# Kernel tuning notes

Hardware: AMD Instinct MI355X
Metric: run time of the kernel (lower is better)

The kernel has to match this reference:

```python
import jax, jax.numpy as jnp
import numpy as np

N_SRC = 50000
N_DST = 50000
N_EDGES = 1600000
D_IN = 128
K = 8          # num_heads
D_OUT = 16     # out_dim per head (K*D_OUT = 128)
NEG_SLOPE = 0.2


def setup_inputs() -> dict:
    key = jax.random.key(0)
    ks = jax.random.split(key, 8)
    feat_src = jax.random.normal(ks[0], (N_SRC, D_IN), dtype=jnp.float32)
    feat_dst = jax.random.normal(ks[1], (N_DST, D_IN), dtype=jnp.float32)
    W_src = jax.random.normal(ks[2], (D_IN, K * D_OUT), dtype=jnp.float32) * (1.0 / np.sqrt(D_IN))
    b_src = jnp.zeros((K * D_OUT,), dtype=jnp.float32)
    W_dst = jax.random.normal(ks[3], (D_IN, K * D_OUT), dtype=jnp.float32) * (1.0 / np.sqrt(D_IN))
    b_dst = jnp.zeros((K * D_OUT,), dtype=jnp.float32)
    attn_src = jax.random.normal(ks[4], (K, 2 * D_OUT), dtype=jnp.float32) * 0.1
    src_idx = jax.random.randint(ks[5], (N_EDGES,), 0, N_SRC, dtype=jnp.int64)
    dst_idx = jax.random.randint(ks[6], (N_EDGES,), 0, N_DST, dtype=jnp.int64)
    return {"feat_src": feat_src, "feat_dst": feat_dst, "W_src": W_src, "b_src": b_src,
            "W_dst": W_dst, "b_dst": b_dst, "attn_src": attn_src,
            "src_idx": src_idx, "dst_idx": dst_idx}


def reference(feat_src, feat_dst, W_src, b_src, W_dst, b_dst, attn_src, src_idx, dst_idx):
    n_dst = feat_dst.shape[0]
    # feat_drop is identity (p=0). Linear projections, reshape to heads.
    hs = (feat_src @ W_src + b_src).reshape(-1, K, D_OUT)  # [N_src, K, D_out]
    hd = (feat_dst @ W_dst + b_dst).reshape(-1, K, D_OUT)  # [N_dst, K, D_out]
    # per-node attention logits
    el = jnp.sum(hs * attn_src[:, :D_OUT], axis=-1)  # [N_src, K]
    er = jnp.sum(hd * attn_src[:, D_OUT:], axis=-1)  # [N_dst, K]
    # per-edge score: u_add_v then LeakyReLU
    e = el[src_idx] + er[dst_idx]                    # [E, K]
    e = jnp.where(e >= 0, e, NEG_SLOPE * e)
    # edge softmax over incoming edges of each dst node (numerically stable)
    emax = jax.ops.segment_max(e, dst_idx, num_segments=n_dst)
    emax = jnp.where(jnp.isfinite(emax), emax, 0.0)  # handle dsts with no edges
    ee = jnp.exp(e - emax[dst_idx])                  # [E, K]
    esum = jax.ops.segment_sum(ee, dst_idx, num_segments=n_dst)
    a = ee / esum[dst_idx]                           # [E, K]
    # weighted message aggregation: u_mul_e then sum over incoming edges
    m = hs[src_idx] * a[:, :, None]                  # [E, K, D_out]
    out = jax.ops.segment_sum(m, dst_idx, num_segments=n_dst)  # [N_dst, K, D_out]
    return out.reshape(n_dst, K * D_OUT)
```

## Files before the change

### kernel.cpp

```cpp
#include <hip/hip_runtime.h>
#include <hip/hip_bf16.h>

#define NEG_SLOPE 0.2f
#define EPB  8192
#define MAXC 2048

typedef __attribute__((ext_vector_type(8))) short bf16x8;
typedef __attribute__((ext_vector_type(4))) float f32x4;

__device__ __forceinline__ float b2f_lo(unsigned u) { return __uint_as_float(u << 16); }
__device__ __forceinline__ float b2f_hi(unsigned u) { return __uint_as_float(u & 0xffff0000u); }

__device__ __forceinline__ short f2b(float x) {
    unsigned u = __float_as_uint(x);
    unsigned r = (u + 0x7fffu + ((u >> 16) & 1u)) >> 16;
    return (short)r;
}

__global__ __launch_bounds__(256) void pack_kernel(
    const float* __restrict__ W_src, const float* __restrict__ W_dst,
    const float* __restrict__ b_src, const float* __restrict__ b_dst,
    const float* __restrict__ attn,
    uint4* __restrict__ wp_src, uint4* __restrict__ wp_dst,
    float* __restrict__ c_all)
{
    const int e = blockIdx.x * 256 + threadIdx.x;
    if (e < 4608) {
        const int which = e / 2304;
        const int e2 = e % 2304;
        const float* W = which ? W_dst : W_src;
        uint4* wp = which ? wp_dst : wp_src;
        const int aoff = which ? 16 : 0;
        short out[8];
        if (e2 < 2048) {
            const int t = e2 >> 8, q = (e2 >> 6) & 3, l = e2 & 63;
            const int kbase = (l >> 4) * 8 + q * 32;
            const int n = t * 16 + (l & 15);
            #pragma unroll
            for (int j = 0; j < 8; ++j) out[j] = f2b(W[(size_t)(kbase + j) * 128 + n]);
            *(uint4*)&wp[(t * 4 + q) * 64 + l] = *(uint4*)out;
        } else {
            const int e3 = e2 - 2048;
            const int q = e3 >> 6, l = e3 & 63;
            const int kbase = (l >> 4) * 8 + q * 32;
            const int n = l & 15;
            #pragma unroll
            for (int j = 0; j < 8; ++j) {
                float v = 0.f;
                if (n < 8) {
                    for (int dd = 0; dd < 16; ++dd)
                        v += W[(size_t)(kbase + j) * 128 + n * 16 + dd] * attn[n * 32 + aoff + dd];
                }
                out[j] = f2b(v);
            }
            *(uint4*)&wp[(32 + q) * 64 + l] = *(uint4*)out;
        }
    } else if (e < 4624) {
        const int k = e - 4608;
        const int which = k >> 3, kk = k & 7;
        const float* bb = which ? b_dst : b_src;
        const int aoff = which ? 16 : 0;
        float v = 0.f;
        for (int dd = 0; dd < 16; ++dd) v += bb[kk * 16 + dd] * attn[kk * 32 + aoff + dd];
        c_all[k] = v;
    }
}

__device__ __forceinline__ void hist_body(
    const int* __restrict__ dst_idx, int* __restrict__ Hmat,
    int nEdges, int nCoarse, int nCB, int bx)
{
    __shared__ int h[MAXC];
    const int t = threadIdx.x;
    for (int i = t; i < nCoarse; i += 256) h[i] = 0;
    __syncthreads();
    const int e0 = bx * EPB;
    const int e1 = min(e0 + EPB, nEdges);
    for (int e = e0 + t; e < e1; e += 256) atomicAdd(&h[dst_idx[e] >> 5], 1);
    __syncthreads();
    for (int i = t; i < nCoarse; i += 256) Hmat[(size_t)i * nCB + bx] = h[i];
}

template<bool STORE_H>
__device__ __forceinline__ void proj_body(
    const float* __restrict__ feat, const uint4* __restrict__ wp,
    const float* __restrict__ b, const float* __restrict__ cvec,
    short* __restrict__ hs_out, float* __restrict__ el_out,
    int N, int bx)
{
    const int t = threadIdx.x;
    const int lane = t & 63;
    const int w = t >> 6;
    const int m  = lane & 15;
    const int q8 = lane >> 4;
    const int row0 = bx * 128 + w * 32;

    f32x4 acc0[9], acc1[9];
    #pragma unroll
    for (int tt = 0; tt < 8; ++tt) {
        const float bn = b[tt * 16 + m];
        acc0[tt] = (f32x4){bn, bn, bn, bn};
        acc1[tt] = (f32x4){bn, bn, bn, bn};
    }
    acc0[8] = (f32x4){0.f, 0.f, 0.f, 0.f};
    acc1[8] = (f32x4){0.f, 0.f, 0.f, 0.f};

    int rowA0 = row0 + m;      if (rowA0 >= N) rowA0 = N - 1;
    int rowA1 = row0 + 16 + m; if (rowA1 >= N) rowA1 = N - 1;
    const float* f0 = feat + (size_t)rowA0 * 128 + q8 * 8;
    const float* f1 = feat + (size_t)rowA1 * 128 + q8 * 8;
    const bf16x8* wpv = (const bf16x8*)wp;

    #pragma unroll
    for (int kc = 0; kc < 4; ++kc) {
        const float4 fa0 = *(const float4*)(f0 + kc * 32);
        const float4 fb0 = *(const float4*)(f0 + kc * 32 + 4);
        const float4 fa1 = *(const float4*)(f1 + kc * 32);
        const float4 fb1 = *(const float4*)(f1 + kc * 32 + 4);
        bf16x8 a0, a1;
        a0[0]=f2b(fa0.x); a0[1]=f2b(fa0.y); a0[2]=f2b(fa0.z); a0[3]=f2b(fa0.w);
        a0[4]=f2b(fb0.x); a0[5]=f2b(fb0.y); a0[6]=f2b(fb0.z); a0[7]=f2b(fb0.w);
        a1[0]=f2b(fa1.x); a1[1]=f2b(fa1.y); a1[2]=f2b(fa1.z); a1[3]=f2b(fa1.w);
        a1[4]=f2b(fb1.x); a1[5]=f2b(fb1.y); a1[6]=f2b(fb1.z); a1[7]=f2b(fb1.w);
        #pragma unroll
        for (int tt = 0; tt < 8; ++tt) {
            const bf16x8 bf = wpv[(tt * 4 + kc) * 64 + lane];
            acc0[tt] = __builtin_amdgcn_mfma_f32_16x16x32_bf16(a0, bf, acc0[tt], 0, 0, 0);
            acc1[tt] = __builtin_amdgcn_mfma_f32_16x16x32_bf16(a1, bf, acc1[tt], 0, 0, 0);
        }
        {
            const bf16x8 bv = wpv[(32 + kc) * 64 + lane];
            acc0[8] = __builtin_amdgcn_mfma_f32_16x16x32_bf16(a0, bv, acc0[8], 0, 0, 0);
            acc1[8] = __builtin_amdgcn_mfma_f32_16x16x32_bf16(a1, bv, acc1[8], 0, 0, 0);
        }
    }

    #pragma unroll
    for (int half = 0; half < 2; ++half) {
        const f32x4* acc = half ? acc1 : acc0;
        const int rbase = row0 + half * 16 + q8 * 4;
        #pragma unroll
        for (int reg = 0; reg < 4; ++reg) {
            const int row = rbase + reg;
            if (row < N) {
                if (STORE_H) {
                    #pragma unroll
                    for (int tt = 0; tt < 8; ++tt)
                        hs_out[(size_t)row * 128 + tt * 16 + m] = f2b(acc[tt][reg]);
                }
                if (m < 8) el_out[(size_t)row * 8 + m] = acc[8][reg] + cvec[m];
            }
        }
    }
}

__global__ __launch_bounds__(256, 2) void fused_proj_hist_kernel(
    const float* __restrict__ feat_src, const float* __restrict__ feat_dst,
    const uint4* __restrict__ wp_src, const uint4* __restrict__ wp_dst,
    const float* __restrict__ b_src, const float* __restrict__ b_dst,
    const float* __restrict__ c_all,
    short* __restrict__ hs, float* __restrict__ el, float* __restrict__ er,
    const int* __restrict__ dst_idx, int* __restrict__ Hmat,
    int n_src, int n_dst, int nEdges, int nCoarse, int nCB, int pSrcBlocks)
{
    int bx = blockIdx.x;
    if (bx < nCB) { hist_body(dst_idx, Hmat, nEdges, nCoarse, nCB, bx); return; }
    bx -= nCB;
    if (bx < pSrcBlocks) {
        proj_body<true>(feat_src, wp_src, b_src, c_all, hs, el, n_src, bx);
        return;
    }
    bx -= pSrcBlocks;
    proj_body<false>(feat_dst, wp_dst, b_dst, c_all + 8, nullptr, er, n_dst, bx);
}

__global__ __launch_bounds__(1024) void scan_part_kernel(
    const int* __restrict__ cnt, int* __restrict__ part, int n)
{
    __shared__ int wsum[16];
    const int t = threadIdx.x;
    const int i = blockIdx.x * 1024 + t;
    int v = (i < n) ? cnt[i] : 0;
    #pragma unroll
    for (int s = 32; s > 0; s >>= 1) v += __shfl_down(v, s, 64);
    if ((t & 63) == 0) wsum[t >> 6] = v;
    __syncthreads();
    if (t < 16) {
        int x = wsum[t];
        #pragma unroll
        for (int s = 8; s > 0; s >>= 1) x += __shfl_down(x, s, 64);
        if (t == 0) part[blockIdx.x] = x;
    }
}

__global__ __launch_bounds__(1024) void scan_top_kernel(
    int* __restrict__ part, int* __restrict__ S, int nPart, int n)
{
    __shared__ int buf[1024];
    const int t = threadIdx.x;
    const int v = (t < nPart) ? part[t] : 0;
    buf[t] = v;
    __syncthreads();
    #pragma unroll
    for (int s = 1; s < 1024; s <<= 1) {
        const int add = (t >= s) ? buf[t - s] : 0;
        __syncthreads();
        buf[t] += add;
        __syncthreads();
    }
    if (t < nPart) part[t] = buf[t] - v;
    if (t == 1023) S[n] = buf[1023];
}

__global__ __launch_bounds__(1024) void scan_local_kernel(
    const int* __restrict__ cnt, const int* __restrict__ part,
    int* __restrict__ S, int n)
{
    __shared__ int buf[1024];
    const int t = threadIdx.x;
    const int i = blockIdx.x * 1024 + t;
    const int v = (i < n) ? cnt[i] : 0;
    buf[t] = v;
    __syncthreads();
    #pragma unroll
    for (int s = 1; s < 1024; s <<= 1) {
        const int add = (t >= s) ? buf[t - s] : 0;
        __syncthreads();
        buf[t] += add;
        __syncthreads();
    }
    if (i < n) S[i] = part[blockIdx.x] + buf[t] - v;
}

__global__ __launch_bounds__(256) void coarse_scatter_kernel(
    const int* __restrict__ src_idx, const int* __restrict__ dst_idx,
    const int* __restrict__ S, int* __restrict__ coarse,
    int nEdges, int nCoarse, int nCB)
{
    __shared__ int base_s[MAXC];
    __shared__ int cur_s[MAXC];
    const int t = threadIdx.x, bx = blockIdx.x;
    for (int i = t; i < nCoarse; i += 256) {
        base_s[i] = S[(size_t)i * nCB + bx];
        cur_s[i]  = 0;
    }
    __syncthreads();
    const int e0 = bx * EPB;
    const int e1 = min(e0 + EPB, nEdges);
    for (int e = e0 + t; e < e1; e += 256) {
        const int d = dst_idx[e];
        const int s = src_idx[e];
        const int bin = d >> 5;
        const int lr = atomicAdd(&cur_s[bin], 1);
        coarse[base_s[bin] + lr] = (s << 5) | (d & 31);
    }
}

__global__ __launch_bounds__(256) void fine_sort_kernel(
    const int* __restrict__ coarse, const int* __restrict__ S,
    int* __restrict__ off, int* __restrict__ sorted_src,
    int nEdges, int n_dst, int nCoarse, int nCB)
{
    __shared__ int h[32];
    __shared__ int cu[32];
    const int t = threadIdx.x, c = blockIdx.x;
    const int base = S[(size_t)c * nCB];
    const int endp = (c + 1 < nCoarse) ? S[(size_t)(c + 1) * nCB] : nEdges;
    if (t < 32) h[t] = 0;
    __syncthreads();
    for (int i = base + t; i < endp; i += 256) atomicAdd(&h[coarse[i] & 31], 1);
    __syncthreads();
    if (t == 0) {
        int run = 0;
        #pragma unroll
        for (int j = 0; j < 32; ++j) {
            cu[j] = run;
            const int d = c * 32 + j;
            if (d < n_dst) off[d] = base + run;
            run += h[j];
        }
    }
    __syncthreads();
    for (int i = base + t; i < endp; i += 256) {
        const int v = coarse[i];
        const int p = atomicAdd(&cu[v & 31], 1);
        sorted_src[base + p] = v >> 5;
    }
    if (c == 0 && t == 0) off[n_dst] = nEdges;
}

__global__ __launch_bounds__(256) void reduce_kernel(
    const int* __restrict__ sorted_src, const int* __restrict__ off,
    const __hip_bfloat16* __restrict__ hs,
    const float* __restrict__ el,
    const float* __restrict__ er,
    float* __restrict__ out,
    int n_dst)
{
    const int wid = blockIdx.x * 4 + (threadIdx.x >> 6);
    if (wid >= n_dst) return;
    const int lane = threadIdx.x & 63;
    const int sub  = lane >> 5;
    const int l32  = lane & 31;
    const int k    = l32 >> 2;
    const float erk = er[(size_t)wid * 8 + k];
    const int beg = off[wid], end = off[wid + 1];

    float a0 = 0.f, a1 = 0.f, a2 = 0.f, a3 = 0.f, es = 0.f;
    int i = beg + sub;
    for (; i + 2 < end; i += 4) {
        const int sA = sorted_src[i];
        const int sB = sorted_src[i + 2];
        const float lA = el[(size_t)sA * 8 + k];
        const float lB = el[(size_t)sB * 8 + k];
        const uint2 uA = ((const uint2*)(hs + (size_t)sA * 128))[l32];
        const uint2 uB = ((const uint2*)(hs + (size_t)sB * 128))[l32];
        float xA = lA + erk; xA = (xA >= 0.f) ? xA : NEG_SLOPE * xA;
        float xB = lB + erk; xB = (xB >= 0.f) ? xB : NEG_SLOPE * xB;
        const float eA = __expf(xA);
        const float eB = __expf(xB);
        es += eA + eB;
        a0 = fmaf(eA, b2f_lo(uA.x), a0); a1 = fmaf(eA, b2f_hi(uA.x), a1);
        a2 = fmaf(eA, b2f_lo(uA.y), a2); a3 = fmaf(eA, b2f_hi(uA.y), a3);
        a0 = fmaf(eB, b2f_lo(uB.x), a0); a1 = fmaf(eB, b2f_hi(uB.x), a1);
        a2 = fmaf(eB, b2f_lo(uB.y), a2); a3 = fmaf(eB, b2f_hi(uB.y), a3);
    }
    for (; i < end; i += 2) {
        const int s = sorted_src[i];
        const float l = el[(size_t)s * 8 + k];
        const uint2 u = ((const uint2*)(hs + (size_t)s * 128))[l32];
        float x = l + erk; x = (x >= 0.f) ? x : NEG_SLOPE * x;
        const float ee = __expf(x);
        es += ee;
        a0 = fmaf(ee, b2f_lo(u.x), a0); a1 = fmaf(ee, b2f_hi(u.x), a1);
        a2 = fmaf(ee, b2f_lo(u.y), a2); a3 = fmaf(ee, b2f_hi(u.y), a3);
    }
    es += __shfl_xor(es, 32);
    a0 += __shfl_xor(a0, 32);
    a1 += __shfl_xor(a1, 32);
    a2 += __shfl_xor(a2, 32);
    a3 += __shfl_xor(a3, 32);
    if (sub == 0) {
        const float inv = (es > 0.f) ? 1.f / es : 0.f;
        float4 o;
        o.x = a0 * inv; o.y = a1 * inv; o.z = a2 * inv; o.w = a3 * inv;
        *(float4*)(out + (size_t)wid * 128 + l32 * 4) = o;
    }
}

extern "C" void kernel_launch(void* const* d_in, const int* in_sizes, int n_in,
                              void* d_out, int out_size, void* d_ws, size_t ws_size,
                              hipStream_t stream) {
    const float* feat_src = (const float*)d_in[0];
    const float* feat_dst = (const float*)d_in[1];
    const float* W_src    = (const float*)d_in[2];
    const float* b_src    = (const float*)d_in[3];
    const float* W_dst    = (const float*)d_in[4];
    const float* b_dst    = (const float*)d_in[5];
    const float* attn     = (const float*)d_in[6];
    const int*   src_idx  = (const int*)d_in[7];
    const int*   dst_idx  = (const int*)d_in[8];
    float* out = (float*)d_out;

    const int n_src  = in_sizes[0] / 128;
    const int n_dst  = in_sizes[1] / 128;
    const int nEdges = in_sizes[7];

    const int nCoarse = (n_dst + 31) >> 5;
    const int nCB     = (nEdges + EPB - 1) / EPB;
    const int nH      = nCoarse * nCB;
    const int nPart   = (nH + 1023) / 1024;
    const int pSrc    = (n_src + 127) / 128;
    const int pDst    = (n_dst + 127) / 128;

    __hip_bfloat16* hs = (__hip_bfloat16*)d_ws;
    float* el   = (float*)(hs + (size_t)n_src * 128);
    float* er   = el + (size_t)n_src * 8;
    int*   off  = (int*)(er + (size_t)n_dst * 8);
    int*   part = off + n_dst + 4;
    int*   Hmat = part + 1024;
    int*   Sarr = Hmat + nH;
    int*   coarse = Sarr + nH + 4;
    int*   sorted_src = coarse + nEdges;
    uintptr_t p = (uintptr_t)(sorted_src + nEdges);
    p = (p + 15) & ~(uintptr_t)15;
    uint4* wp_src = (uint4*)p;
    uint4* wp_dst = wp_src + 36 * 64;
    float* c_all  = (float*)(wp_dst + 36 * 64);

    pack_kernel<<<19, 256, 0, stream>>>(W_src, W_dst, b_src, b_dst, attn,
                                        wp_src, wp_dst, c_all);

    fused_proj_hist_kernel<<<nCB + pSrc + pDst, 256, 0, stream>>>(
        feat_src, feat_dst, wp_src, wp_dst, b_src, b_dst, c_all,
        (short*)hs, el, er, dst_idx, Hmat,
        n_src, n_dst, nEdges, nCoarse, nCB, pSrc);

    scan_part_kernel<<<nPart, 1024, 0, stream>>>(Hmat, part, nH);
    scan_top_kernel<<<1, 1024, 0, stream>>>(part, Sarr, nPart, nH);
    scan_local_kernel<<<nPart, 1024, 0, stream>>>(Hmat, part, Sarr, nH);

    coarse_scatter_kernel<<<nCB, 256, 0, stream>>>(src_idx, dst_idx, Sarr,
                                                   coarse, nEdges, nCoarse, nCB);
    fine_sort_kernel<<<nCoarse, 256, 0, stream>>>(coarse, Sarr, off, sorted_src,
                                                  nEdges, n_dst, nCoarse, nCB);

    reduce_kernel<<<(n_dst + 3) / 4, 256, 0, stream>>>(sorted_src, off, hs, el, er, out, n_dst);
}
```

Before: 248.5 us.

## Precompute per-edge attention weights in fine sort, store as fp16

Moves the LeakyReLU and exp for every edge and head into the fine-sort kernel, which writes an fp16 weight array of 8 values per edge next to the sorted source list. The reduce kernel then reads the contiguous weights instead of gathering el by source and recomputing exp. This cuts random gathers and exp work in the reduce, but adds 16 bytes per edge of writes plus reads and an el gather inside the sort kernel. fp16 storage of unnormalized exp values risks precision loss or overflow when logits are large.

```diff
diff --git a/kernel.cpp b/kernel.cpp
--- a/kernel.cpp
+++ b/kernel.cpp
@@ -1,5 +1,6 @@
 #include <hip/hip_runtime.h>
 #include <hip/hip_bf16.h>
+#include <hip/hip_fp16.h>
 
 #define NEG_SLOPE 0.2f
 #define EPB  8192
@@ -258,15 +259,23 @@
 
 __global__ __launch_bounds__(256) void fine_sort_kernel(
     const int* __restrict__ coarse, const int* __restrict__ S,
+    const float* __restrict__ el,
+    const float* __restrict__ er,
     int* __restrict__ off, int* __restrict__ sorted_src,
+    unsigned short* __restrict__ pw,
     int nEdges, int n_dst, int nCoarse, int nCB)
 {
     __shared__ int h[32];
     __shared__ int cu[32];
+    __shared__ float erL[32 * 8];
     const int t = threadIdx.x, c = blockIdx.x;
     const int base = S[(size_t)c * nCB];
     const int endp = (c + 1 < nCoarse) ? S[(size_t)(c + 1) * nCB] : nEdges;
     if (t < 32) h[t] = 0;
+    {
+        const int d = c * 32 + (t >> 3);
+        erL[t] = (d < n_dst) ? er[(size_t)d * 8 + (t & 7)] : 0.f;
+    }
     __syncthreads();
     for (int i = base + t; i < endp; i += 256) atomicAdd(&h[coarse[i] & 31], 1);
     __syncthreads();
@@ -283,17 +292,30 @@
     __syncthreads();
     for (int i = base + t; i < endp; i += 256) {
         const int v = coarse[i];
-        const int p = atomicAdd(&cu[v & 31], 1);
-        sorted_src[base + p] = v >> 5;
+        const int d = v & 31;
+        const int s = v >> 5;
+        const int p = atomicAdd(&cu[d], 1);
+        sorted_src[base + p] = s;
+        const float4 e0 = *(const float4*)(el + (size_t)s * 8);
+        const float4 e1 = *(const float4*)(el + (size_t)s * 8 + 4);
+        const float xs[8] = {e0.x, e0.y, e0.z, e0.w, e1.x, e1.y, e1.z, e1.w};
+        unsigned short w[8];
+        #pragma unroll
+        for (int k = 0; k < 8; ++k) {
+            float x = xs[k] + erL[d * 8 + k];
+            x = (x >= 0.f) ? x : NEG_SLOPE * x;
+            const __half hw = __float2half(__expf(x));
+            w[k] = __half_as_ushort(hw);
+        }
+        *(uint4*)(pw + (size_t)(base + p) * 8) = *(uint4*)w;
     }
     if (c == 0 && t == 0) off[n_dst] = nEdges;
 }
 
 __global__ __launch_bounds__(256) void reduce_kernel(
     const int* __restrict__ sorted_src, const int* __restrict__ off,
-    const __hip_bfloat16* __restrict__ hs,
-    const float* __restrict__ el,
-    const float* __restrict__ er,
+    const unsigned short* __restrict__ hs,
+    const unsigned short* __restrict__ pw,
     float* __restrict__ out,
     int n_dst)
 {
@@ -303,7 +325,8 @@
     const int sub  = lane >> 5;
     const int l32  = lane & 31;
     const int k    = l32 >> 2;
-    const float erk = er[(size_t)wid * 8 + k];
+    const int k2   = k & 6;
+    const int khi  = k & 1;
     const int beg = off[wid], end = off[wid + 1];
 
     float a0 = 0.f, a1 = 0.f, a2 = 0.f, a3 = 0.f, es = 0.f;
@@ -311,14 +334,14 @@
     for (; i + 2 < end; i += 4) {
         const int sA = sorted_src[i];
         const int sB = sorted_src[i + 2];
-        const float lA = el[(size_t)sA * 8 + k];
-        const float lB = el[(size_t)sB * 8 + k];
+        const unsigned wpA = *(const unsigned*)(pw + (size_t)i * 8 + k2);
+        const unsigned wpB = *(const unsigned*)(pw + (size_t)(i + 2) * 8 + k2);
         const uint2 uA = ((const uint2*)(hs + (size_t)sA * 128))[l32];
         const uint2 uB = ((const uint2*)(hs + (size_t)sB * 128))[l32];
-        float xA = lA + erk; xA = (xA >= 0.f) ? xA : NEG_SLOPE * xA;
-        float xB = lB + erk; xB = (xB >= 0.f) ? xB : NEG_SLOPE * xB;
-        const float eA = __expf(xA);
-        const float eB = __expf(xB);
+        const unsigned short usA = khi ? (unsigned short)(wpA >> 16) : (unsigned short)(wpA & 0xffff);
+        const unsigned short usB = khi ? (unsigned short)(wpB >> 16) : (unsigned short)(wpB & 0xffff);
+        const float eA = __half2float(__ushort_as_half(usA));
+        const float eB = __half2float(__ushort_as_half(usB));
         es += eA + eB;
         a0 = fmaf(eA, b2f_lo(uA.x), a0); a1 = fmaf(eA, b2f_hi(uA.x), a1);
         a2 = fmaf(eA, b2f_lo(uA.y), a2); a3 = fmaf(eA, b2f_hi(uA.y), a3);
@@ -327,10 +350,10 @@
     }
     for (; i < end; i += 2) {
         const int s = sorted_src[i];
-        const float l = el[(size_t)s * 8 + k];
+        const unsigned wp4 = *(const unsigned*)(pw + (size_t)i * 8 + k2);
         const uint2 u = ((const uint2*)(hs + (size_t)s * 128))[l32];
-        float x = l + erk; x = (x >= 0.f) ? x : NEG_SLOPE * x;
-        const float ee = __expf(x);
+        const unsigned short us = khi ? (unsigned short)(wp4 >> 16) : (unsigned short)(wp4 & 0xffff);
+        const float ee = __half2float(__ushort_as_half(us));
         es += ee;
         a0 = fmaf(ee, b2f_lo(u.x), a0); a1 = fmaf(ee, b2f_hi(u.x), a1);
         a2 = fmaf(ee, b2f_lo(u.y), a2); a3 = fmaf(ee, b2f_hi(u.y), a3);
@@ -382,7 +405,8 @@
     int*   Sarr = Hmat + nH;
     int*   coarse = Sarr + nH + 4;
     int*   sorted_src = coarse + nEdges;
-    uintptr_t p = (uintptr_t)(sorted_src + nEdges);
+    unsigned short* pw = (unsigned short*)(sorted_src + nEdges);
+    uintptr_t p = (uintptr_t)(pw + (size_t)nEdges * 8);
     p = (p + 15) & ~(uintptr_t)15;
     uint4* wp_src = (uint4*)p;
     uint4* wp_dst = wp_src + 36 * 64;
@@ -402,8 +426,10 @@
 
     coarse_scatter_kernel<<<nCB, 256, 0, stream>>>(src_idx, dst_idx, Sarr,
                                                    coarse, nEdges, nCoarse, nCB);
-    fine_sort_kernel<<<nCoarse, 256, 0, stream>>>(coarse, Sarr, off, sorted_src,
+    fine_sort_kernel<<<nCoarse, 256, 0, stream>>>(coarse, Sarr, el, er,
+                                                  off, sorted_src, pw,
                                                   nEdges, n_dst, nCoarse, nCB);
 
-    reduce_kernel<<<(n_dst + 3) / 4, 256, 0, stream>>>(sorted_src, off, hs, el, er, out, n_dst);
-}
+    reduce_kernel<<<(n_dst + 3) / 4, 256, 0, stream>>>(sorted_src, off,
+        (const unsigned short*)hs, pw, out, n_dst);
+}
```

After: 259.6 us. 1.04x slower.
